# Kernel tuning notes

Hardware: AMD Instinct MI355X
Metric: run time of the kernel (lower is better)

The kernel has to match this reference:

```python
import jax, jax.numpy as jnp
import numpy as np

N_NODES = 50000
N_EDGES = 1600000
HIDDEN = 64
N_BLOCKS = 2
N_ITERS = 2


def setup_inputs() -> dict:
    key = jax.random.key(0)
    ks = jax.random.split(key, 10)
    hidden = jax.random.normal(ks[0], (N_NODES, HIDDEN), dtype=jnp.float32)
    src = jax.random.randint(ks[1], (N_EDGES,), 0, N_NODES)
    dst = jax.random.randint(ks[2], (N_EDGES,), 0, N_NODES)
    s = 0.05  # keep MLP activations well-scaled
    W1 = jax.random.normal(ks[3], (N_BLOCKS, 3 * HIDDEN, 128), dtype=jnp.float32) * s
    b1 = jax.random.normal(ks[4], (N_BLOCKS, 128), dtype=jnp.float32) * s
    W2 = jax.random.normal(ks[5], (N_BLOCKS, 128, 128), dtype=jnp.float32) * s
    b2 = jax.random.normal(ks[6], (N_BLOCKS, 128), dtype=jnp.float32) * s
    W3 = jax.random.normal(ks[7], (N_BLOCKS, 128, HIDDEN), dtype=jnp.float32) * s
    b3 = jax.random.normal(ks[8], (N_BLOCKS, HIDDEN), dtype=jnp.float32) * s
    return {"hidden": hidden, "src": src, "dst": dst,
            "W1": W1, "b1": b1, "W2": W2, "b2": b2, "W3": W3, "b3": b3}


def _node_update(hidden, src, dst, w1, c1, w2, c2, w3, c3):
    # global rep: sum of all node hidden reps, broadcast to every node
    grep = jnp.broadcast_to(jnp.sum(hidden, axis=0, keepdims=True), hidden.shape)
    # mailbox sum: gather src features, segment-sum into dst
    msgs = hidden[src]                                  # [E, H]
    agg = jax.ops.segment_sum(msgs, dst, num_segments=hidden.shape[0])  # [N, H]
    x = jnp.concatenate([agg, hidden, grep], axis=1)    # [N, 3H]
    h = jax.nn.relu(x @ w1 + c1)
    h = jax.nn.relu(h @ w2 + c2)
    out = h @ w3 + c3
    # row-wise L2 (fro over dim=1) normalization
    norm = jnp.sqrt(jnp.sum(out * out, axis=1, keepdims=True))
    return out / norm


def reference(hidden, src, dst, W1, b1, W2, b2, W3, b3):
    for blk in range(N_BLOCKS):
        for _ in range(N_ITERS):
            hidden = _node_update(hidden, src, dst,
                                  W1[blk], b1[blk], W2[blk], b2[blk], W3[blk], b3[blk])
    return hidden
```

## Files before the change

### kernel.cpp

```cpp
#include <hip/hip_runtime.h>
#include <math.h>

#define NN 50000
#define NE 1600000
#define H  64

#define SHIFT 7
#define NPBKT 128
#define NB    391
#define CHUNK 4096
#define NCH   391

typedef __attribute__((ext_vector_type(8))) short s16v8;
typedef __attribute__((ext_vector_type(4))) float f32v4;
typedef __attribute__((ext_vector_type(8))) _Float16 f16v8;
typedef unsigned short u16;
typedef unsigned int   u32;

__device__ __forceinline__ u16 f2bf(float x) {
    union { float f; unsigned u; } v; v.f = x;
    unsigned r = v.u + 0x7FFF + ((v.u >> 16) & 1);
    return (u16)(r >> 16);
}
__device__ __forceinline__ float bf2f(u16 h) {
    union { float f; unsigned u; } v; v.u = ((unsigned)h) << 16; return v.f;
}

__global__ __launch_bounds__(256) void hist_kernel(const int* __restrict__ dst,
                                                   int* __restrict__ chunkhist) {
    __shared__ int h[NB];
    const int c = blockIdx.x;
    for (int b = threadIdx.x; b < NB; b += 256) h[b] = 0;
    __syncthreads();
    const int e0 = c * CHUNK, e1 = min(NE, e0 + CHUNK);
    for (int e = e0 + threadIdx.x; e < e1; e += 256)
        atomicAdd(&h[dst[e] >> SHIFT], 1);
    __syncthreads();
    for (int b = threadIdx.x; b < NB; b += 256)
        chunkhist[c * NB + b] = h[b];
}

__global__ __launch_bounds__(512) void cscan_kernel(int* __restrict__ chunkhist,
                                                    int* __restrict__ bbase) {
    __shared__ int s[512];
    const int t = threadIdx.x;
    int tot = 0;
    if (t < NB)
        for (int c = 0; c < NCH; ++c) tot += chunkhist[c * NB + t];
    s[t] = (t < NB) ? tot : 0;
    __syncthreads();
    for (int d = 1; d < 512; d <<= 1) {
        int v = (t >= d) ? s[t - d] : 0;
        __syncthreads();
        s[t] += v;
        __syncthreads();
    }
    if (t < NB) {
        int base = s[t] - tot;
        bbase[t] = base;
        if (t == NB - 1) bbase[NB] = s[t];
        int run = base;
        for (int c = 0; c < NCH; ++c) {
            int tmp = chunkhist[c * NB + t];
            chunkhist[c * NB + t] = run;
            run += tmp;
        }
    }
}

__global__ __launch_bounds__(256) void scat_kernel(const int* __restrict__ src,
                                                   const int* __restrict__ dst,
                                                   const int* __restrict__ chunkhist,
                                                   u32* __restrict__ bin) {
    __shared__ int base[NB];
    __shared__ int cur[NB];
    const int c = blockIdx.x;
    for (int b = threadIdx.x; b < NB; b += 256) {
        base[b] = chunkhist[c * NB + b];
        cur[b] = 0;
    }
    __syncthreads();
    const int e0 = c * CHUNK, e1 = min(NE, e0 + CHUNK);
    for (int e = e0 + threadIdx.x; e < e1; e += 256) {
        int d = dst[e];
        int b = d >> SHIFT;
        int p = atomicAdd(&cur[b], 1);
        bin[base[b] + p] = (u32)src[e] | ((u32)(d & (NPBKT - 1)) << 16);
    }
}

__global__ __launch_bounds__(256) void binB_kernel(const u32* __restrict__ bin,
                                                   const int* __restrict__ bbase,
                                                   int* __restrict__ off,
                                                   u16* __restrict__ csr) {
    __shared__ int deg[NPBKT];
    __shared__ int sc[NPBKT];
    __shared__ int cur[NPBKT];
    const int b = blockIdx.x, t = threadIdx.x;
    const int seg0 = bbase[b], seg1 = bbase[b + 1];
    if (t < NPBKT) { deg[t] = 0; cur[t] = 0; }
    __syncthreads();
    for (int i = seg0 + t; i < seg1; i += 256)
        atomicAdd(&deg[(bin[i] >> 16) & (NPBKT - 1)], 1);
    __syncthreads();
    if (t < NPBKT) sc[t] = deg[t];
    __syncthreads();
    for (int d = 1; d < NPBKT; d <<= 1) {
        int v = 0;
        if (t < NPBKT && t >= d) v = sc[t - d];
        __syncthreads();
        if (t < NPBKT) sc[t] += v;
        __syncthreads();
    }
    if (t < NPBKT) {
        sc[t] -= deg[t];
        int node = b * NPBKT + t;
        if (node < NN) off[node] = seg0 + sc[t];
        if (b == 0 && t == 0) off[NN] = NE;
    }
    __syncthreads();
    for (int i = seg0 + t; i < seg1; i += 256) {
        u32 e = bin[i];
        int n = (e >> 16) & (NPBKT - 1);
        int p = atomicAdd(&cur[n], 1);
        csr[seg0 + sc[n] + p] = (u16)(e & 0xFFFF);
    }
}

__global__ __launch_bounds__(256) void prep_kernel(const float* __restrict__ W1,
        const float* __restrict__ W2, const float* __restrict__ W3,
        u16* __restrict__ wt) {
    int idx = blockIdx.x * 256 + threadIdx.x;
    if (idx >= 2 * 40960) return;
    int b = idx / 40960, r = idx - b * 40960;
    float v; int hioff, losz;
    if (r < 16384) {
        int col = r >> 7, k = r & 127;
        v = W1[b * 24576 + k * 128 + col];
        hioff = b * 81920 + r; losz = 16384;
    } else if (r < 32768) {
        int rr = r - 16384; int col = rr >> 7, k = rr & 127;
        v = W2[b * 16384 + k * 128 + col];
        hioff = b * 81920 + 32768 + rr; losz = 16384;
    } else {
        int rr = r - 32768; int col = rr >> 7, k = rr & 127;
        v = W3[b * 8192 + k * 64 + col];
        hioff = b * 81920 + 65536 + rr; losz = 8192;
    }
    u16 hi = f2bf(v);
    u16 lo = f2bf(v - bf2f(hi));
    wt[hioff] = hi; wt[hioff + losz] = lo;
}

__global__ __launch_bounds__(256) void grep_kernel(const float* __restrict__ h,
                                                   float* __restrict__ partial,
                                                   _Float16* __restrict__ h16) {
    const int c  = threadIdx.x & 63;
    const int rl = threadIdx.x >> 6;
    float acc = 0.f;
    for (int r = blockIdx.x * 4 + rl; r < NN; r += gridDim.x * 4) {
        float v = h[r * H + c];
        h16[r * H + c] = (_Float16)v;
        acc += v;
    }
    __shared__ float s[4][64];
    s[rl][c] = acc;
    __syncthreads();
    if (threadIdx.x < 64)
        partial[blockIdx.x * 64 + threadIdx.x] =
            s[0][threadIdx.x] + s[1][threadIdx.x] +
            s[2][threadIdx.x] + s[3][threadIdx.x];
}

__global__ __launch_bounds__(1024) void b1e_kernel(const float* __restrict__ partial,
        int nparts,
        const float* __restrict__ W1, const float* __restrict__ b1,
        float* __restrict__ b1e) {
    __shared__ float sg[16][64];
    __shared__ float g[64];
    const int t = threadIdx.x;
    const int c = t & 63, rl = t >> 6;
    float s = 0.f;
    for (int i = rl; i < nparts; i += 16) s += partial[i * 64 + c];
    sg[rl][c] = s;
    __syncthreads();
    if (t < 64) {
        float a = 0.f;
#pragma unroll
        for (int j = 0; j < 16; ++j) a += sg[j][t];
        g[t] = a;
    }
    __syncthreads();
    if (t < 128) {
        float s2 = b1[t];
        for (int k = 0; k < 64; ++k)
            s2 = fmaf(g[k], W1[(128 + k) * 128 + t], s2);
        b1e[t] = s2;
    }
}

__global__ __launch_bounds__(256) void gather_kernel(const _Float16* __restrict__ h16,
                                                     const u16* __restrict__ csr,
                                                     const int* __restrict__ off,
                                                     float* __restrict__ agg) {
    const int wid = blockIdx.x * 4 + (threadIdx.x >> 6);
    if (wid >= NN) return;
    const int lane = threadIdx.x & 63;
    const int g8 = lane >> 3, sub = lane & 7;
    const int beg = off[wid], end = off[wid + 1];
    float a[8] = {0.f, 0.f, 0.f, 0.f, 0.f, 0.f, 0.f, 0.f};
    for (int e = beg + g8; e < end; e += 8) {
        int s = csr[e];
        f16v8 v = *(const f16v8*)&h16[(size_t)s * 64 + sub * 8];
#pragma unroll
        for (int j = 0; j < 8; ++j) a[j] += (float)v[j];
    }
#pragma unroll
    for (int o = 8; o <= 32; o <<= 1) {
#pragma unroll
        for (int j = 0; j < 8; ++j) a[j] += __shfl_xor(a[j], o);
    }
    if (g8 == 0) {
        float4 v0 = {a[0], a[1], a[2], a[3]};
        float4 v1 = {a[4], a[5], a[6], a[7]};
        *(float4*)&agg[(size_t)wid * 64 + sub * 8] = v0;
        *(float4*)&agg[(size_t)wid * 64 + sub * 8 + 4] = v1;
    }
}

#define MLP_MFMA(d, a, b) d = __builtin_amdgcn_mfma_f32_16x16x32_bf16(a, b, d, 0, 0, 0)

__global__ __launch_bounds__(512, 4) void mlp_mfma(
    const float* __restrict__ agg, const float* __restrict__ hin,
    const float* __restrict__ b1e, const u16* __restrict__ wt,
    const float* __restrict__ b2, const float* __restrict__ b3,
    float* __restrict__ out, _Float16* __restrict__ h16out,
    float* __restrict__ colpart)
{
    __shared__ u16 xhi[64 * 128], xlo[64 * 128];
    __shared__ u16 hhi[64 * 128], hlo[64 * 128];
    __shared__ float ssw[4][64];
    __shared__ float colp[64];
    const int t = threadIdx.x;
    const int wl = t >> 6, lane = t & 63;
    const int li = lane & 15, g = lane >> 4;
    const int n0 = blockIdx.x * 64;

    const u16* w1hi = wt;
    const u16* w1lo = wt + 16384;
    const u16* w2hi = wt + 32768;
    const u16* w2lo = wt + 49152;
    const u16* w3hi = wt + 65536;
    const u16* w3lo = wt + 73728;

    {
        const int row = t >> 3, col0 = (t & 7) * 16;
        const int node = min(n0 + row, NN - 1);
        const float* sp = (col0 < 64) ? (agg + (size_t)node * 64 + col0)
                                      : (hin + (size_t)node * 64 + (col0 - 64));
        float4 u0 = *(const float4*)sp;
        float4 u1 = *(const float4*)(sp + 4);
        float4 u2 = *(const float4*)(sp + 8);
        float4 u3 = *(const float4*)(sp + 12);
        float f[16] = {u0.x, u0.y, u0.z, u0.w, u1.x, u1.y, u1.z, u1.w,
                       u2.x, u2.y, u2.z, u2.w, u3.x, u3.y, u3.z, u3.w};
        s16v8 hv0, lv0, hv1, lv1;
#pragma unroll
        for (int j = 0; j < 8; ++j) {
            u16 hb = f2bf(f[j]);
            hv0[j] = (short)hb;
            lv0[j] = (short)f2bf(f[j] - bf2f(hb));
            u16 hb1 = f2bf(f[8 + j]);
            hv1[j] = (short)hb1;
            lv1[j] = (short)f2bf(f[8 + j] - bf2f(hb1));
        }
        const int cb = col0 >> 3;
        const int a0 = row * 128 + (((cb ^ (row & 7)) << 3));
        const int a1 = row * 128 + ((((cb + 1) ^ (row & 7)) << 3));
        *(s16v8*)&xhi[a0] = hv0; *(s16v8*)&xlo[a0] = lv0;
        *(s16v8*)&xhi[a1] = hv1; *(s16v8*)&xlo[a1] = lv1;
    }
    __syncthreads();

    {
        const int col = wl * 16 + li;
        s16v8 Bh[4], Bl[4];
#pragma unroll
        for (int ks = 0; ks < 4; ++ks) {
            Bh[ks] = *(const s16v8*)(w1hi + col * 128 + ks * 32 + g * 8);
            Bl[ks] = *(const s16v8*)(w1lo + col * 128 + ks * 32 + g * 8);
        }
        f32v4 acc[4];
#pragma unroll
        for (int i = 0; i < 4; ++i) acc[i] = (f32v4){0.f, 0.f, 0.f, 0.f};
#pragma unroll
        for (int rt = 0; rt < 4; ++rt) {
            const int row = rt * 16 + li;
#pragma unroll
            for (int ks = 0; ks < 4; ++ks) {
                const int kb = ks * 4 + g;
                const int addr = row * 128 + ((kb ^ (row & 7)) << 3);
                s16v8 Ah = *(const s16v8*)&xhi[addr];
                s16v8 Al = *(const s16v8*)&xlo[addr];
                MLP_MFMA(acc[rt], Ah, Bh[ks]);
                MLP_MFMA(acc[rt], Ah, Bl[ks]);
                MLP_MFMA(acc[rt], Al, Bh[ks]);
            }
        }
        const float bb = b1e[col];
        const int cb = col >> 3, c7 = col & 7;
#pragma unroll
        for (int rt = 0; rt < 4; ++rt) {
#pragma unroll
            for (int r = 0; r < 4; ++r) {
                float hv = fmaxf(acc[rt][r] + bb, 0.f);
                u16 hb = f2bf(hv);
                u16 lb = f2bf(hv - bf2f(hb));
                const int row = rt * 16 + g * 4 + r;
                const int addr = row * 128 + (((cb ^ (row & 7)) << 3) | c7);
                hhi[addr] = hb; hlo[addr] = lb;
            }
        }
    }
    __syncthreads();

    {
        const int col = wl * 16 + li;
        s16v8 Bh[4], Bl[4];
#pragma unroll
        for (int ks = 0; ks < 4; ++ks) {
            Bh[ks] = *(const s16v8*)(w2hi + col * 128 + ks * 32 + g * 8);
            Bl[ks] = *(const s16v8*)(w2lo + col * 128 + ks * 32 + g * 8);
        }
        f32v4 acc[4];
#pragma unroll
        for (int i = 0; i < 4; ++i) acc[i] = (f32v4){0.f, 0.f, 0.f, 0.f};
#pragma unroll
        for (int rt = 0; rt < 4; ++rt) {
            const int row = rt * 16 + li;
#pragma unroll
            for (int ks = 0; ks < 4; ++ks) {
                const int kb = ks * 4 + g;
                const int addr = row * 128 + ((kb ^ (row & 7)) << 3);
                s16v8 Ah = *(const s16v8*)&hhi[addr];
                s16v8 Al = *(const s16v8*)&hlo[addr];
                MLP_MFMA(acc[rt], Ah, Bh[ks]);
                MLP_MFMA(acc[rt], Ah, Bl[ks]);
                MLP_MFMA(acc[rt], Al, Bh[ks]);
            }
        }
        const float bb = b2[col];
        const int cb = col >> 3, c7 = col & 7;
#pragma unroll
        for (int rt = 0; rt < 4; ++rt) {
#pragma unroll
            for (int r = 0; r < 4; ++r) {
                float hv = fmaxf(acc[rt][r] + bb, 0.f);
                u16 hb = f2bf(hv);
                u16 lb = f2bf(hv - bf2f(hb));
                const int row = rt * 16 + g * 4 + r;
                const int addr = row * 128 + (((cb ^ (row & 7)) << 3) | c7);
                xhi[addr] = hb; xlo[addr] = lb;
            }
        }
    }
    __syncthreads();

    float v[4][4];
    if (wl < 4) {
        const int col = wl * 16 + li;
        s16v8 Bh[4], Bl[4];
#pragma unroll
        for (int ks = 0; ks < 4; ++ks) {
            Bh[ks] = *(const s16v8*)(w3hi + col * 128 + ks * 32 + g * 8);
            Bl[ks] = *(const s16v8*)(w3lo + col * 128 + ks * 32 + g * 8);
        }
        f32v4 acc[4];
#pragma unroll
        for (int i = 0; i < 4; ++i) acc[i] = (f32v4){0.f, 0.f, 0.f, 0.f};
#pragma unroll
        for (int rt = 0; rt < 4; ++rt) {
            const int row = rt * 16 + li;
#pragma unroll
            for (int ks = 0; ks < 4; ++ks) {
                const int kb = ks * 4 + g;
                const int addr = row * 128 + ((kb ^ (row & 7)) << 3);
                s16v8 Ah = *(const s16v8*)&xhi[addr];
                s16v8 Al = *(const s16v8*)&xlo[addr];
                MLP_MFMA(acc[rt], Ah, Bh[ks]);
                MLP_MFMA(acc[rt], Ah, Bl[ks]);
                MLP_MFMA(acc[rt], Al, Bh[ks]);
            }
        }
        const float bb = b3[col];
#pragma unroll
        for (int rt = 0; rt < 4; ++rt) {
#pragma unroll
            for (int r = 0; r < 4; ++r) {
                float vv = acc[rt][r] + bb;
                v[rt][r] = vv;
                float s2 = vv * vv;
#pragma unroll
                for (int o = 1; o <= 8; o <<= 1) s2 += __shfl_xor(s2, o);
                if (li == 0) ssw[wl][rt * 16 + g * 4 + r] = s2;
            }
        }
    }
    __syncthreads();
    if (wl < 4) {
        const int col = wl * 16 + li;
        float cs = 0.f;
#pragma unroll
        for (int rt = 0; rt < 4; ++rt) {
#pragma unroll
            for (int r = 0; r < 4; ++r) {
                const int row = rt * 16 + g * 4 + r;
                const float tot = ssw[0][row] + ssw[1][row] +
                                  ssw[2][row] + ssw[3][row];
                const float inv = rsqrtf(tot);
                const int node = n0 + row;
                float ov = v[rt][r] * inv;
                if (node < NN) {
                    out[(size_t)node * 64 + col] = ov;
                    h16out[(size_t)node * 64 + col] = (_Float16)ov;
                    cs += ov;
                }
            }
        }
        cs += __shfl_xor(cs, 16);
        cs += __shfl_xor(cs, 32);
        if (g == 0) colp[col] = cs;
    }
    __syncthreads();
    if (t < 64)
        colpart[(size_t)blockIdx.x * 64 + t] = colp[t];
}

extern "C" void kernel_launch(void* const* d_in, const int* in_sizes, int n_in,
                              void* d_out, int out_size, void* d_ws, size_t ws_size,
                              hipStream_t stream) {
    const float* hidden = (const float*)d_in[0];
    const int*   src    = (const int*)d_in[1];
    const int*   dst    = (const int*)d_in[2];
    const float* W1f    = (const float*)d_in[3];
    const float* b1f    = (const float*)d_in[4];
    const float* W2f    = (const float*)d_in[5];
    const float* b2f    = (const float*)d_in[6];
    const float* W3f    = (const float*)d_in[7];
    const float* b3f    = (const float*)d_in[8];

    const int NBLK = (NN + 63) / 64;

    float* agg     = (float*)d_ws;
    float* b1e     = agg + (size_t)NN * H;
    float* partA   = b1e + 128;
    float* partB   = partA + 256 * 64;
    float* hA      = partB + (size_t)NBLK * 64;
    int*   bbase   = (int*)(hA + (size_t)NN * H);
    int*   off     = bbase + (NB + 1);
    int*   chist   = off + (NN + 1);
    u32*   bin     = (u32*)(chist + NCH * NB);
    u16*   csr     = (u16*)(bin + NE);
    u16*   wt      = (u16*)(((uintptr_t)(csr + NE) + 255) & ~(uintptr_t)255);
    _Float16* h16  = (_Float16*)(wt + 2 * 81920);

    hist_kernel<<<NCH, 256, 0, stream>>>(dst, chist);
    cscan_kernel<<<1, 512, 0, stream>>>(chist, bbase);
    scat_kernel<<<NCH, 256, 0, stream>>>(src, dst, chist, bin);
    binB_kernel<<<NB, 256, 0, stream>>>(bin, bbase, off, csr);
    prep_kernel<<<(2 * 40960 + 255) / 256, 256, 0, stream>>>(W1f, W2f, W3f, wt);

    grep_kernel<<<256, 256, 0, stream>>>(hidden, partA, h16);

    const float* hin = hidden;
    float* houts[4] = { hA, (float*)d_out, hA, (float*)d_out };

    for (int it = 0; it < 4; ++it) {
        const int blk = it >> 1;
        const float* part = (it == 0) ? partA : partB;
        const int nparts  = (it == 0) ? 256 : NBLK;
        b1e_kernel<<<1, 1024, 0, stream>>>(part, nparts,
            W1f + blk * 24576, b1f + blk * 128, b1e);
        gather_kernel<<<(NN + 3) / 4, 256, 0, stream>>>(h16, csr, off, agg);
        mlp_mfma<<<NBLK, 512, 0, stream>>>(agg, hin, b1e, wt + blk * 81920,
            b2f + blk * 128, b3f + blk * 64, houts[it], h16, partB);
        hin = houts[it];
    }
}
```

Baseline: 417.7 us.

## Fuse neighbor gather into MLP kernel with ping-pong fp16 buffers

Removes the separate gather kernel and the fp32 agg buffer. Each MLP block now gathers neighbor features for its own 64 nodes directly from the fp16 hidden copy into shared memory. The x staging buffers are dropped and a single hhi/hlo pair is reused, with extra barriers placed before each in-place overwrite. Two fp16 buffers alternate so a block never reads features that are being rewritten in the same pass. The gather now uses one 8-lane group per node instead of a full wavefront, which may reduce memory-level parallelism for high-degree nodes. Smaller LDS use could raise occupancy.

```diff
diff --git a/kernel.cpp b/kernel.cpp
--- a/kernel.cpp
+++ b/kernel.cpp
@@ -199,45 +199,16 @@
     }
 }
 
-__global__ __launch_bounds__(256) void gather_kernel(const _Float16* __restrict__ h16,
-                                                     const u16* __restrict__ csr,
-                                                     const int* __restrict__ off,
-                                                     float* __restrict__ agg) {
-    const int wid = blockIdx.x * 4 + (threadIdx.x >> 6);
-    if (wid >= NN) return;
-    const int lane = threadIdx.x & 63;
-    const int g8 = lane >> 3, sub = lane & 7;
-    const int beg = off[wid], end = off[wid + 1];
-    float a[8] = {0.f, 0.f, 0.f, 0.f, 0.f, 0.f, 0.f, 0.f};
-    for (int e = beg + g8; e < end; e += 8) {
-        int s = csr[e];
-        f16v8 v = *(const f16v8*)&h16[(size_t)s * 64 + sub * 8];
-#pragma unroll
-        for (int j = 0; j < 8; ++j) a[j] += (float)v[j];
-    }
-#pragma unroll
-    for (int o = 8; o <= 32; o <<= 1) {
-#pragma unroll
-        for (int j = 0; j < 8; ++j) a[j] += __shfl_xor(a[j], o);
-    }
-    if (g8 == 0) {
-        float4 v0 = {a[0], a[1], a[2], a[3]};
-        float4 v1 = {a[4], a[5], a[6], a[7]};
-        *(float4*)&agg[(size_t)wid * 64 + sub * 8] = v0;
-        *(float4*)&agg[(size_t)wid * 64 + sub * 8 + 4] = v1;
-    }
-}
-
 #define MLP_MFMA(d, a, b) d = __builtin_amdgcn_mfma_f32_16x16x32_bf16(a, b, d, 0, 0, 0)
 
-__global__ __launch_bounds__(512, 4) void mlp_mfma(
-    const float* __restrict__ agg, const float* __restrict__ hin,
+__global__ __launch_bounds__(512, 4) void fused_mlp(
+    const _Float16* __restrict__ h16in, const float* __restrict__ hin,
     const float* __restrict__ b1e, const u16* __restrict__ wt,
     const float* __restrict__ b2, const float* __restrict__ b3,
+    const u16* __restrict__ csr, const int* __restrict__ off,
     float* __restrict__ out, _Float16* __restrict__ h16out,
     float* __restrict__ colpart)
 {
-    __shared__ u16 xhi[64 * 128], xlo[64 * 128];
     __shared__ u16 hhi[64 * 128], hlo[64 * 128];
     __shared__ float ssw[4][64];
     __shared__ float colp[64];
@@ -254,31 +225,54 @@
     const u16* w3lo = wt + 73728;
 
     {
-        const int row = t >> 3, col0 = (t & 7) * 16;
+        const int nl = lane >> 3, sub = lane & 7;
+        const int node = min(n0 + wl * 8 + nl, NN - 1);
+        const int beg = off[node], end = off[node + 1];
+        float a[8] = {0.f, 0.f, 0.f, 0.f, 0.f, 0.f, 0.f, 0.f};
+        int e = beg;
+        for (; e + 1 < end; e += 2) {
+            const int s0 = csr[e], s1 = csr[e + 1];
+            f16v8 v0 = *(const f16v8*)&h16in[(size_t)s0 * 64 + sub * 8];
+            f16v8 v1 = *(const f16v8*)&h16in[(size_t)s1 * 64 + sub * 8];
+#pragma unroll
+            for (int j = 0; j < 8; ++j) a[j] += (float)v0[j] + (float)v1[j];
+        }
+        if (e < end) {
+            const int s0 = csr[e];
+            f16v8 v0 = *(const f16v8*)&h16in[(size_t)s0 * 64 + sub * 8];
+#pragma unroll
+            for (int j = 0; j < 8; ++j) a[j] += (float)v0[j];
+        }
+        const int row = wl * 8 + nl;
+        s16v8 hv, lv;
+#pragma unroll
+        for (int j = 0; j < 8; ++j) {
+            u16 hb = f2bf(a[j]);
+            hv[j] = (short)hb;
+            lv[j] = (short)f2bf(a[j] - bf2f(hb));
+        }
+        const int addr = row * 128 + ((sub ^ (row & 7)) << 3);
+        *(s16v8*)&hhi[addr] = hv;
+        *(s16v8*)&hlo[addr] = lv;
+    }
+    {
+        const int row = t >> 3, c8 = t & 7;
         const int node = min(n0 + row, NN - 1);
-        const float* sp = (col0 < 64) ? (agg + (size_t)node * 64 + col0)
-                                      : (hin + (size_t)node * 64 + (col0 - 64));
+        const float* sp = hin + (size_t)node * 64 + c8 * 8;
         float4 u0 = *(const float4*)sp;
         float4 u1 = *(const float4*)(sp + 4);
-        float4 u2 = *(const float4*)(sp + 8);
-        float4 u3 = *(const float4*)(sp + 12);
-        float f[16] = {u0.x, u0.y, u0.z, u0.w, u1.x, u1.y, u1.z, u1.w,
-                       u2.x, u2.y, u2.z, u2.w, u3.x, u3.y, u3.z, u3.w};
-        s16v8 hv0, lv0, hv1, lv1;
+        float f[8] = {u0.x, u0.y, u0.z, u0.w, u1.x, u1.y, u1.z, u1.w};
+        s16v8 hv, lv;
 #pragma unroll
         for (int j = 0; j < 8; ++j) {
             u16 hb = f2bf(f[j]);
-            hv0[j] = (short)hb;
-            lv0[j] = (short)f2bf(f[j] - bf2f(hb));
-            u16 hb1 = f2bf(f[8 + j]);
-            hv1[j] = (short)hb1;
-            lv1[j] = (short)f2bf(f[8 + j] - bf2f(hb1));
-        }
-        const int cb = col0 >> 3;
-        const int a0 = row * 128 + (((cb ^ (row & 7)) << 3));
-        const int a1 = row * 128 + ((((cb + 1) ^ (row & 7)) << 3));
-        *(s16v8*)&xhi[a0] = hv0; *(s16v8*)&xlo[a0] = lv0;
-        *(s16v8*)&xhi[a1] = hv1; *(s16v8*)&xlo[a1] = lv1;
+            hv[j] = (short)hb;
+            lv[j] = (short)f2bf(f[j] - bf2f(hb));
+        }
+        const int cb = 8 + c8;
+        const int addr = row * 128 + ((cb ^ (row & 7)) << 3);
+        *(s16v8*)&hhi[addr] = hv;
+        *(s16v8*)&hlo[addr] = lv;
     }
     __syncthreads();
 
@@ -289,48 +283,6 @@
         for (int ks = 0; ks < 4; ++ks) {
             Bh[ks] = *(const s16v8*)(w1hi + col * 128 + ks * 32 + g * 8);
             Bl[ks] = *(const s16v8*)(w1lo + col * 128 + ks * 32 + g * 8);
-        }
-        f32v4 acc[4];
-#pragma unroll
-        for (int i = 0; i < 4; ++i) acc[i] = (f32v4){0.f, 0.f, 0.f, 0.f};
-#pragma unroll
-        for (int rt = 0; rt < 4; ++rt) {
-            const int row = rt * 16 + li;
-#pragma unroll
-            for (int ks = 0; ks < 4; ++ks) {
-                const int kb = ks * 4 + g;
-                const int addr = row * 128 + ((kb ^ (row & 7)) << 3);
-                s16v8 Ah = *(const s16v8*)&xhi[addr];
-                s16v8 Al = *(const s16v8*)&xlo[addr];
-                MLP_MFMA(acc[rt], Ah, Bh[ks]);
-                MLP_MFMA(acc[rt], Ah, Bl[ks]);
-                MLP_MFMA(acc[rt], Al, Bh[ks]);
-            }
-        }
-        const float bb = b1e[col];
-        const int cb = col >> 3, c7 = col & 7;
-#pragma unroll
-        for (int rt = 0; rt < 4; ++rt) {
-#pragma unroll
-            for (int r = 0; r < 4; ++r) {
-                float hv = fmaxf(acc[rt][r] + bb, 0.f);
-                u16 hb = f2bf(hv);
-                u16 lb = f2bf(hv - bf2f(hb));
-                const int row = rt * 16 + g * 4 + r;
-                const int addr = row * 128 + (((cb ^ (row & 7)) << 3) | c7);
-                hhi[addr] = hb; hlo[addr] = lb;
-            }
-        }
-    }
-    __syncthreads();
-
-    {
-        const int col = wl * 16 + li;
-        s16v8 Bh[4], Bl[4];
-#pragma unroll
-        for (int ks = 0; ks < 4; ++ks) {
-            Bh[ks] = *(const s16v8*)(w2hi + col * 128 + ks * 32 + g * 8);
-            Bl[ks] = *(const s16v8*)(w2lo + col * 128 + ks * 32 + g * 8);
         }
         f32v4 acc[4];
 #pragma unroll
@@ -349,7 +301,8 @@
                 MLP_MFMA(acc[rt], Al, Bh[ks]);
             }
         }
-        const float bb = b2[col];
+        __syncthreads();
+        const float bb = b1e[col];
         const int cb = col >> 3, c7 = col & 7;
 #pragma unroll
         for (int rt = 0; rt < 4; ++rt) {
@@ -360,7 +313,50 @@
                 u16 lb = f2bf(hv - bf2f(hb));
                 const int row = rt * 16 + g * 4 + r;
                 const int addr = row * 128 + (((cb ^ (row & 7)) << 3) | c7);
-                xhi[addr] = hb; xlo[addr] = lb;
+                hhi[addr] = hb; hlo[addr] = lb;
+            }
+        }
+    }
+    __syncthreads();
+
+    {
+        const int col = wl * 16 + li;
+        s16v8 Bh[4], Bl[4];
+#pragma unroll
+        for (int ks = 0; ks < 4; ++ks) {
+            Bh[ks] = *(const s16v8*)(w2hi + col * 128 + ks * 32 + g * 8);
+            Bl[ks] = *(const s16v8*)(w2lo + col * 128 + ks * 32 + g * 8);
+        }
+        f32v4 acc[4];
+#pragma unroll
+        for (int i = 0; i < 4; ++i) acc[i] = (f32v4){0.f, 0.f, 0.f, 0.f};
+#pragma unroll
+        for (int rt = 0; rt < 4; ++rt) {
+            const int row = rt * 16 + li;
+#pragma unroll
+            for (int ks = 0; ks < 4; ++ks) {
+                const int kb = ks * 4 + g;
+                const int addr = row * 128 + ((kb ^ (row & 7)) << 3);
+                s16v8 Ah = *(const s16v8*)&hhi[addr];
+                s16v8 Al = *(const s16v8*)&hlo[addr];
+                MLP_MFMA(acc[rt], Ah, Bh[ks]);
+                MLP_MFMA(acc[rt], Ah, Bl[ks]);
+                MLP_MFMA(acc[rt], Al, Bh[ks]);
+            }
+        }
+        __syncthreads();
+        const float bb = b2[col];
+        const int cb = col >> 3, c7 = col & 7;
+#pragma unroll
+        for (int rt = 0; rt < 4; ++rt) {
+#pragma unroll
+            for (int r = 0; r < 4; ++r) {
+                float hv = fmaxf(acc[rt][r] + bb, 0.f);
+                u16 hb = f2bf(hv);
+                u16 lb = f2bf(hv - bf2f(hb));
+                const int row = rt * 16 + g * 4 + r;
+                const int addr = row * 128 + (((cb ^ (row & 7)) << 3) | c7);
+                hhi[addr] = hb; hlo[addr] = lb;
             }
         }
     }
@@ -385,8 +381,8 @@
             for (int ks = 0; ks < 4; ++ks) {
                 const int kb = ks * 4 + g;
                 const int addr = row * 128 + ((kb ^ (row & 7)) << 3);
-                s16v8 Ah = *(const s16v8*)&xhi[addr];
-                s16v8 Al = *(const s16v8*)&xlo[addr];
+                s16v8 Ah = *(const s16v8*)&hhi[addr];
+                s16v8 Al = *(const s16v8*)&hlo[addr];
                 MLP_MFMA(acc[rt], Ah, Bh[ks]);
                 MLP_MFMA(acc[rt], Ah, Bl[ks]);
                 MLP_MFMA(acc[rt], Al, Bh[ks]);
@@ -451,8 +447,7 @@
 
     const int NBLK = (NN + 63) / 64;
 
-    float* agg     = (float*)d_ws;
-    float* b1e     = agg + (size_t)NN * H;
+    float* b1e     = (float*)d_ws;
     float* partA   = b1e + 128;
     float* partB   = partA + 256 * 64;
     float* hA      = partB + (size_t)NBLK * 64;
@@ -462,7 +457,8 @@
     u32*   bin     = (u32*)(chist + NCH * NB);
     u16*   csr     = (u16*)(bin + NE);
     u16*   wt      = (u16*)(((uintptr_t)(csr + NE) + 255) & ~(uintptr_t)255);
-    _Float16* h16  = (_Float16*)(wt + 2 * 81920);
+    _Float16* h16a = (_Float16*)(wt + 2 * 81920);
+    _Float16* h16b = h16a + (size_t)NN * H;
 
     hist_kernel<<<NCH, 256, 0, stream>>>(dst, chist);
     cscan_kernel<<<1, 512, 0, stream>>>(chist, bbase);
@@ -470,10 +466,11 @@
     binB_kernel<<<NB, 256, 0, stream>>>(bin, bbase, off, csr);
     prep_kernel<<<(2 * 40960 + 255) / 256, 256, 0, stream>>>(W1f, W2f, W3f, wt);
 
-    grep_kernel<<<256, 256, 0, stream>>>(hidden, partA, h16);
+    grep_kernel<<<256, 256, 0, stream>>>(hidden, partA, h16a);
 
     const float* hin = hidden;
     float* houts[4] = { hA, (float*)d_out, hA, (float*)d_out };
+    _Float16* h16bufs[2] = { h16a, h16b };
 
     for (int it = 0; it < 4; ++it) {
         const int blk = it >> 1;
@@ -481,9 +478,10 @@
         const int nparts  = (it == 0) ? 256 : NBLK;
         b1e_kernel<<<1, 1024, 0, stream>>>(part, nparts,
             W1f + blk * 24576, b1f + blk * 128, b1e);
-        gather_kernel<<<(NN + 3) / 4, 256, 0, stream>>>(h16, csr, off, agg);
-        mlp_mfma<<<NBLK, 512, 0, stream>>>(agg, hin, b1e, wt + blk * 81920,
-            b2f + blk * 128, b3f + blk * 64, houts[it], h16, partB);
+        fused_mlp<<<NBLK, 512, 0, stream>>>(
+            h16bufs[it & 1], hin, b1e, wt + blk * 81920,
+            b2f + blk * 128, b3f + blk * 64, csr, off,
+            houts[it], h16bufs[(it + 1) & 1], partB);
         hin = houts[it];
     }
 }
```

Measured after the change: 409.5 us. 1.02x faster.
